# Kernel tuning notes

Hardware: AMD Instinct MI355X
Metric: run time of the kernel (lower is better)

## Reference

```python
import jax, jax.numpy as jnp
import numpy as np

SOFTASSIGN_LAYERS = 10  # MTSPSoftassign layers
EPS = 1e-8


def softassign(output):
    # output: (b, m, n, n)
    b, m, n, _ = output.shape
    # stabilizing max-subtraction (layers > 0 branch)
    depots_max = jnp.max(output[:, :, :1, :], axis=3, keepdims=True)            # (b,m,1,1)
    others_max = jnp.max(output[:, :, 1:, :], axis=(1, 3), keepdims=True)       # (b,1,n-1,1)
    output_max = jnp.concatenate([
        jnp.broadcast_to(depots_max, (b, m, 1, n)),
        jnp.broadcast_to(others_max, (b, m, n - 1, n)),
    ], axis=2)
    output = jnp.exp(output - output_max)
    for _ in range(SOFTASSIGN_LAYERS):
        output = jnp.maximum(output, EPS)
        starts = output[:, :, :1, :]
        starts = starts / jnp.sum(starts, axis=3, keepdims=True)                # normalize_dims (3,)
        nexts = output[:, :, 1:, :]
        nexts = nexts / jnp.sum(nexts, axis=(1, 3), keepdims=True)              # normalize_dims (1,3)
        output = jnp.swapaxes(jnp.concatenate([starts, nexts], axis=2), 2, 3)
    if SOFTASSIGN_LAYERS % 2 != 0:
        output = jnp.swapaxes(output, 2, 3)
    return output


def setup_inputs() -> dict:
    key = jax.random.key(0)
    ks = jax.random.split(key, 4)
    b, m, n, d = 4, 8, 128, 64
    cities = jax.random.normal(ks[0], (b, n, d), dtype=jnp.float32)
    groups = jax.random.normal(ks[1], (b, m, d), dtype=jnp.float32)
    W1 = jax.random.normal(ks[2], (3 * d, d), dtype=jnp.float32) * 0.05
    b1 = jnp.zeros((d,), dtype=jnp.float32)
    W2 = jax.random.normal(ks[3], (d, 1), dtype=jnp.float32) * 0.05
    b2 = jnp.zeros((1,), dtype=jnp.float32)
    return {"cities": cities, "groups": groups, "W1": W1, "b1": b1, "W2": W2, "b2": b2}


def reference(cities, groups, W1, b1, W2, b2):
    # cities: (b, n, d) embedded city features; groups: (b, m, d) embedded group features.
    # Torch builds nodes = cat(at_groups, from_cities, to_cities) of shape (b,m,n,n,3d)
    # then Linear(3d->d). Linear on a concat == sum of linears on the pieces, so we
    # project each piece once and broadcast-add, avoiding the (b,m,n,n,3d) materialization.
    d = cities.shape[-1]
    Wg, Wf, Wt = W1[:d], W1[d:2 * d], W1[2 * d:]
    hg = jnp.einsum('bmd,de->bme', groups, Wg)   # at_groups projection
    hf = jnp.einsum('bnd,de->bne', cities, Wf)   # from_cities projection
    ht = jnp.einsum('bnd,de->bne', cities, Wt)   # to_cities projection
    h = hg[:, :, None, None, :] + hf[:, None, :, None, :] + ht[:, None, None, :, :] + b1  # (b,m,n,n,d)
    h = jax.nn.relu(h)
    out = jnp.einsum('bmfte,eo->bmfto', h, W2)[..., 0] + b2[0]  # (b,m,n,n)
    return softassign(out)
```

## Files before the change

kernel.cpp:

```cpp
#include <hip/hip_runtime.h>
#include <math.h>

#define EPSF 1e-8f

__device__ __forceinline__ void atomicMaxFloat(float* addr, float val) {
    if (val >= 0.f) atomicMax((int*)addr, __float_as_int(val));
    else            atomicMin((unsigned int*)addr, __float_as_uint(val));
}

__global__ __launch_bounds__(256) void prep_kernel(
        const float* __restrict__ cities, const float* __restrict__ groups,
        const float* __restrict__ W1,
        float* __restrict__ hg, float* __restrict__ hf, float* __restrict__ htT,
        float* __restrict__ S, float* __restrict__ Mbuf,
        unsigned* __restrict__ cnt) {
    int blk = blockIdx.x, tid = threadIdx.x;
    if (blk < 128) {
        int gid = blk * 256 + tid;
        int e = gid & 63;
        int f = (gid >> 6) & 127;
        int b = gid >> 13;
        const float* crow = cities + (b * 128 + f) * 64;
        float af = 0.f, at = 0.f;
        #pragma unroll 8
        for (int d = 0; d < 64; ++d) {
            float c = crow[d];
            af = fmaf(c, W1[(64  + d) * 64 + e], af);
            at = fmaf(c, W1[(128 + d) * 64 + e], at);
        }
        hf [(b * 128 + f) * 64 + e] = af;
        htT[(b * 64  + e) * 128 + f] = at;
    } else if (blk < 136) {
        int gid = (blk - 128) * 256 + tid;
        int e = gid & 63;
        int m = (gid >> 6) & 7;
        int b = gid >> 9;
        const float* grow = groups + (b * 8 + m) * 64;
        float a = 0.f;
        #pragma unroll 8
        for (int d = 0; d < 64; ++d)
            a = fmaf(grow[d], W1[d * 64 + e], a);
        hg[(b * 8 + m) * 64 + e] = a;
    } else {
        for (int i = tid; i < 5120; i += 256) S[i] = 0.f;
        for (int i = tid; i < 544;  i += 256) Mbuf[i] = -INFINITY;
        if (tid < 40) cnt[tid] = 0u;
    }
}

__global__ __launch_bounds__(256) void mlp_kernel(
        const float* __restrict__ hg, const float* __restrict__ hf,
        const float* __restrict__ htT,
        const float* __restrict__ b1, const float* __restrict__ W2,
        const float* __restrict__ b2,
        float* __restrict__ X, float* __restrict__ Mdep, float* __restrict__ Moth) {
    int blk = blockIdx.x;
    int fg  = blk & 15;
    int bm  = blk >> 4;
    int b   = bm >> 3;
    int tid = threadIdx.x;

    __shared__ float hts[64][128];
    __shared__ float arowT[64][8];
    __shared__ float w2s[64];
    __shared__ float wmax[4][4];

    {
        const float4* src = (const float4*)(htT + b * 8192);
        float4* dst = (float4*)(&hts[0][0]);
        #pragma unroll
        for (int i = 0; i < 8; ++i) dst[tid + 256 * i] = src[tid + 256 * i];
    }
    #pragma unroll
    for (int j = 0; j < 2; ++j) {
        int v = tid + 256 * j;
        int e = v >> 3, f8 = v & 7;
        int f = fg * 8 + f8;
        arowT[e][f8] = hg[bm * 64 + e] + hf[(b * 128 + f) * 64 + e] + b1[e];
    }
    if (tid < 64) w2s[tid] = W2[tid];
    __syncthreads();

    int t  = tid & 127;
    int fo = tid >> 7;
    float acc[4] = {0.f, 0.f, 0.f, 0.f};
    #pragma unroll 8
    for (int e = 0; e < 64; ++e) {
        float ht = hts[e][t];
        float w2 = w2s[e];
        float4 ar = *(const float4*)(&arowT[e][fo * 4]);
        acc[0] = fmaf(fmaxf(ar.x + ht, 0.f), w2, acc[0]);
        acc[1] = fmaf(fmaxf(ar.y + ht, 0.f), w2, acc[1]);
        acc[2] = fmaf(fmaxf(ar.z + ht, 0.f), w2, acc[2]);
        acc[3] = fmaf(fmaxf(ar.w + ht, 0.f), w2, acc[3]);
    }

    float b2v = b2[0];
    float fmax4[4];
    #pragma unroll
    for (int i = 0; i < 4; ++i) {
        float out = acc[i] + b2v;
        int f = fg * 8 + fo * 4 + i;
        X[(bm * 128 + f) * 128 + t] = out;
        fmax4[i] = out;
    }

    #pragma unroll
    for (int i = 0; i < 4; ++i)
        #pragma unroll
        for (int off = 32; off; off >>= 1)
            fmax4[i] = fmaxf(fmax4[i], __shfl_down(fmax4[i], off));
    int wv = tid >> 6;
    if ((tid & 63) == 0) {
        #pragma unroll
        for (int i = 0; i < 4; ++i) wmax[wv][i] = fmax4[i];
    }
    __syncthreads();
    if (tid < 8) {
        int w0 = (tid >> 2) * 2, i = tid & 3;
        float m = fmaxf(wmax[w0][i], wmax[w0 + 1][i]);
        int f = fg * 8 + tid;
        if (f == 0) atomicMaxFloat(&Mdep[bm], m);
        else        atomicMaxFloat(&Moth[b * 128 + f], m);
    }
}

__global__ __launch_bounds__(1024) void softassign_kernel(
        float* __restrict__ X, const float* __restrict__ Mdep,
        const float* __restrict__ Moth, float* __restrict__ S,
        unsigned* __restrict__ cnt) {
    int blk = blockIdx.x;
    int b = blk >> 3;
    int tid = threadIdx.x;
    int tf = tid >> 5, tt = tid & 31;
    float* base = X + blk * 16384;

    float x[4][4];
    #pragma unroll
    for (int r = 0; r < 4; ++r) {
        float4 v = *(const float4*)(base + (4 * tf + r) * 128 + 4 * tt);
        x[r][0] = v.x; x[r][1] = v.y; x[r][2] = v.z; x[r][3] = v.w;
    }

    float mdep = Mdep[blk];
    #pragma unroll
    for (int r = 0; r < 4; ++r) {
        int f = 4 * tf + r;
        float M = (f == 0) ? mdep : Moth[b * 128 + f];
        #pragma unroll
        for (int c = 0; c < 4; ++c) x[r][c] = expf(x[r][c] - M);
    }

    __shared__ float part[128][33];
    __shared__ float dnm[128];
    __shared__ float depot;

    for (int k = 0; k < 10; ++k) {
        #pragma unroll
        for (int r = 0; r < 4; ++r)
            #pragma unroll
            for (int c = 0; c < 4; ++c) x[r][c] = fmaxf(x[r][c], EPSF);

        int dir = k & 1;
        if (dir == 0) {
            #pragma unroll
            for (int r = 0; r < 4; ++r)
                part[4 * tf + r][tt] = x[r][0] + x[r][1] + x[r][2] + x[r][3];
        } else {
            #pragma unroll
            for (int c = 0; c < 4; ++c)
                part[4 * tt + c][tf] = x[0][c] + x[1][c] + x[2][c] + x[3][c];
        }
        __syncthreads();
        float* Scur = &S[(k * 4 + b) * 128];
        if (tid < 128) {
            float s = 0.f;
            #pragma unroll 8
            for (int j = 0; j < 32; ++j) s += part[tid][j];
            if (tid == 0) depot = s;
            else atomicAdd(&Scur[tid], s);
        }
        __syncthreads();
        unsigned* ccur = &cnt[k * 4 + b];
        if (tid == 0) {
            __hip_atomic_fetch_add(ccur, 1u, __ATOMIC_RELAXED,
                                   __HIP_MEMORY_SCOPE_AGENT);
            while (__hip_atomic_load(ccur, __ATOMIC_RELAXED,
                                     __HIP_MEMORY_SCOPE_AGENT) < 8u)
                __builtin_amdgcn_s_sleep(1);
        }
        __syncthreads();

        if (tid < 128) {
            dnm[tid] = (tid == 0) ? depot
                : __hip_atomic_load(&Scur[tid], __ATOMIC_RELAXED,
                                    __HIP_MEMORY_SCOPE_AGENT);
        }
        __syncthreads();

        if (dir == 0) {
            #pragma unroll
            for (int r = 0; r < 4; ++r) {
                float inv = 1.f / dnm[4 * tf + r];
                #pragma unroll
                for (int c = 0; c < 4; ++c) x[r][c] *= inv;
            }
        } else {
            #pragma unroll
            for (int c = 0; c < 4; ++c) {
                float inv = 1.f / dnm[4 * tt + c];
                #pragma unroll
                for (int r = 0; r < 4; ++r) x[r][c] *= inv;
            }
        }
    }

    #pragma unroll
    for (int r = 0; r < 4; ++r) {
        float4 v = make_float4(x[r][0], x[r][1], x[r][2], x[r][3]);
        *(float4*)(base + (4 * tf + r) * 128 + 4 * tt) = v;
    }
}

extern "C" void kernel_launch(void* const* d_in, const int* in_sizes, int n_in,
                              void* d_out, int out_size, void* d_ws, size_t ws_size,
                              hipStream_t stream) {
    const float* cities = (const float*)d_in[0];
    const float* groups = (const float*)d_in[1];
    const float* W1     = (const float*)d_in[2];
    const float* b1     = (const float*)d_in[3];
    const float* W2     = (const float*)d_in[4];
    const float* b2     = (const float*)d_in[5];
    float* X  = (float*)d_out;
    float* ws = (float*)d_ws;

    float*    hg   = ws;
    float*    hf   = ws + 2048;
    float*    htT  = ws + 34816;
    float*    S    = ws + 67584;
    float*    Mbuf = ws + 72704;
    float*    Mdep = Mbuf;
    float*    Moth = Mbuf + 32;
    unsigned* cnt  = (unsigned*)(ws + 73248);

    prep_kernel<<<137, 256, 0, stream>>>(cities, groups, W1, hg, hf, htT,
                                         S, Mbuf, cnt);
    mlp_kernel<<<512, 256, 0, stream>>>(hg, hf, htT, b1, W2, b2, X, Mdep, Moth);
    softassign_kernel<<<32, 1024, 0, stream>>>(X, Mdep, Moth, S, cnt);
}
```

Before: 103.2 us.

## Replace atomic-add plus counter barrier with per-block slots polled for nonzero

The cross-block column-sum reduction no longer does atomicAdd into a shared sum followed by a counter-based spin barrier. Each of the 8 blocks per batch now stores its partial sums into its own slot. Each thread then polls all 8 slots until every one is nonzero and sums them locally, which removes the atomic contention and the extra barrier round. To support this, the workspace is enlarged and zeroed by more prep blocks using float4 stores. The approach relies on partial sums never being exactly zero, which holds because entries are clamped to at least EPS.

```diff
diff --git a/kernel.cpp b/kernel.cpp
--- a/kernel.cpp
+++ b/kernel.cpp
@@ -12,8 +12,7 @@
         const float* __restrict__ cities, const float* __restrict__ groups,
         const float* __restrict__ W1,
         float* __restrict__ hg, float* __restrict__ hf, float* __restrict__ htT,
-        float* __restrict__ S, float* __restrict__ Mbuf,
-        unsigned* __restrict__ cnt) {
+        float* __restrict__ S, float* __restrict__ Mbuf) {
     int blk = blockIdx.x, tid = threadIdx.x;
     if (blk < 128) {
         int gid = blk * 256 + tid;
@@ -42,9 +41,15 @@
             a = fmaf(grow[d], W1[d * 64 + e], a);
         hg[(b * 8 + m) * 64 + e] = a;
     } else {
-        for (int i = tid; i < 5120; i += 256) S[i] = 0.f;
-        for (int i = tid; i < 544;  i += 256) Mbuf[i] = -INFINITY;
-        if (tid < 40) cnt[tid] = 0u;
+        int zb = blk - 136;
+        float4 z = make_float4(0.f, 0.f, 0.f, 0.f);
+        float4* S4 = (float4*)S;
+        #pragma unroll
+        for (int i = 0; i < 5; ++i) S4[zb * 1280 + 256 * i + tid] = z;
+        if (zb == 7 && tid < 136) {
+            float ninf = -INFINITY;
+            ((float4*)Mbuf)[tid] = make_float4(ninf, ninf, ninf, ninf);
+        }
     }
 }
 
@@ -127,10 +132,9 @@
 
 __global__ __launch_bounds__(1024) void softassign_kernel(
         float* __restrict__ X, const float* __restrict__ Mdep,
-        const float* __restrict__ Moth, float* __restrict__ S,
-        unsigned* __restrict__ cnt) {
+        const float* __restrict__ Moth, float* __restrict__ S) {
     int blk = blockIdx.x;
-    int b = blk >> 3;
+    int b = blk >> 3, m = blk & 7;
     int tid = threadIdx.x;
     int tf = tid >> 5, tt = tid & 31;
     float* base = X + blk * 16384;
@@ -153,7 +157,6 @@
 
     __shared__ float part[128][33];
     __shared__ float dnm[128];
-    __shared__ float depot;
 
     for (int k = 0; k < 10; ++k) {
         #pragma unroll
@@ -172,29 +175,34 @@
                 part[4 * tt + c][tf] = x[0][c] + x[1][c] + x[2][c] + x[3][c];
         }
         __syncthreads();
-        float* Scur = &S[(k * 4 + b) * 128];
         if (tid < 128) {
             float s = 0.f;
             #pragma unroll 8
             for (int j = 0; j < 32; ++j) s += part[tid][j];
-            if (tid == 0) depot = s;
-            else atomicAdd(&Scur[tid], s);
-        }
-        __syncthreads();
-        unsigned* ccur = &cnt[k * 4 + b];
-        if (tid == 0) {
-            __hip_atomic_fetch_add(ccur, 1u, __ATOMIC_RELAXED,
-                                   __HIP_MEMORY_SCOPE_AGENT);
-            while (__hip_atomic_load(ccur, __ATOMIC_RELAXED,
-                                     __HIP_MEMORY_SCOPE_AGENT) < 8u)
-                __builtin_amdgcn_s_sleep(1);
-        }
-        __syncthreads();
-
-        if (tid < 128) {
-            dnm[tid] = (tid == 0) ? depot
-                : __hip_atomic_load(&Scur[tid], __ATOMIC_RELAXED,
-                                    __HIP_MEMORY_SCOPE_AGENT);
+            if (tid == 0) {
+                dnm[0] = s;
+            } else {
+                float* Scur = S + (k * 4 + b) * 1024;
+                __hip_atomic_store(&Scur[m * 128 + tid], s,
+                                   __ATOMIC_RELAXED, __HIP_MEMORY_SCOPE_AGENT);
+                float tot;
+                for (;;) {
+                    float v[8]; bool ready = true;
+                    #pragma unroll
+                    for (int j = 0; j < 8; ++j)
+                        v[j] = __hip_atomic_load(&Scur[j * 128 + tid],
+                                 __ATOMIC_RELAXED, __HIP_MEMORY_SCOPE_AGENT);
+                    #pragma unroll
+                    for (int j = 0; j < 8; ++j) ready &= (v[j] != 0.f);
+                    if (ready) {
+                        tot = ((v[0] + v[1]) + (v[2] + v[3]))
+                            + ((v[4] + v[5]) + (v[6] + v[7]));
+                        break;
+                    }
+                    __builtin_amdgcn_s_sleep(1);
+                }
+                dnm[tid] = tot;
+            }
         }
         __syncthreads();
 
@@ -234,17 +242,16 @@
     float* X  = (float*)d_out;
     float* ws = (float*)d_ws;
 
-    float*    hg   = ws;
-    float*    hf   = ws + 2048;
-    float*    htT  = ws + 34816;
-    float*    S    = ws + 67584;
-    float*    Mbuf = ws + 72704;
-    float*    Mdep = Mbuf;
-    float*    Moth = Mbuf + 32;
-    unsigned* cnt  = (unsigned*)(ws + 73248);
-
-    prep_kernel<<<137, 256, 0, stream>>>(cities, groups, W1, hg, hf, htT,
-                                         S, Mbuf, cnt);
+    float* hg   = ws;
+    float* hf   = ws + 2048;
+    float* htT  = ws + 34816;
+    float* S    = ws + 67584;
+    float* Mbuf = ws + 108544;
+    float* Mdep = Mbuf;
+    float* Moth = Mbuf + 32;
+
+    prep_kernel<<<144, 256, 0, stream>>>(cities, groups, W1, hg, hf, htT,
+                                         S, Mbuf);
     mlp_kernel<<<512, 256, 0, stream>>>(hg, hf, htT, b1, W2, b2, X, Mdep, Moth);
-    softassign_kernel<<<32, 1024, 0, stream>>>(X, Mdep, Moth, S, cnt);
-}
+    softassign_kernel<<<32, 1024, 0, stream>>>(X, Mdep, Moth, S);
+}
```

New measurement: 99.10 us. -4.0%, faster.

## Reformulate softassign as Sinkhorn scaling vectors over compressed column sums

Applied to the files above, without the earlier changes.

Sinkhorn normalization is rewritten as per-row and per-column scaling factors. Only reduced summaries of exp(X) enter the iterations: column sums over m for non-depot rows, plus the depot row and column per group. A single block per batch runs the ten iterations entirely in shared memory, and a final scale kernel applies the factors to X. This removes the max-subtraction atomics, the cross-block spin-wait barriers and the per-iteration global atomics. In exchange it drops the max stabilization and the EPS clamp, which risks overflow or a change in numerics on other inputs.

```diff
diff --git a/kernel.cpp b/kernel.cpp
--- a/kernel.cpp
+++ b/kernel.cpp
@@ -1,19 +1,10 @@
 #include <hip/hip_runtime.h>
 #include <math.h>
-
-#define EPSF 1e-8f
-
-__device__ __forceinline__ void atomicMaxFloat(float* addr, float val) {
-    if (val >= 0.f) atomicMax((int*)addr, __float_as_int(val));
-    else            atomicMin((unsigned int*)addr, __float_as_uint(val));
-}
 
 __global__ __launch_bounds__(256) void prep_kernel(
         const float* __restrict__ cities, const float* __restrict__ groups,
         const float* __restrict__ W1,
-        float* __restrict__ hg, float* __restrict__ hf, float* __restrict__ htT,
-        float* __restrict__ S, float* __restrict__ Mbuf,
-        unsigned* __restrict__ cnt) {
+        float* __restrict__ hg, float* __restrict__ hf, float* __restrict__ htT) {
     int blk = blockIdx.x, tid = threadIdx.x;
     if (blk < 128) {
         int gid = blk * 256 + tid;
@@ -30,7 +21,7 @@
         }
         hf [(b * 128 + f) * 64 + e] = af;
         htT[(b * 64  + e) * 128 + f] = at;
-    } else if (blk < 136) {
+    } else {
         int gid = (blk - 128) * 256 + tid;
         int e = gid & 63;
         int m = (gid >> 6) & 7;
@@ -41,10 +32,6 @@
         for (int d = 0; d < 64; ++d)
             a = fmaf(grow[d], W1[d * 64 + e], a);
         hg[(b * 8 + m) * 64 + e] = a;
-    } else {
-        for (int i = tid; i < 5120; i += 256) S[i] = 0.f;
-        for (int i = tid; i < 544;  i += 256) Mbuf[i] = -INFINITY;
-        if (tid < 40) cnt[tid] = 0u;
     }
 }
 
@@ -53,7 +40,7 @@
         const float* __restrict__ htT,
         const float* __restrict__ b1, const float* __restrict__ W2,
         const float* __restrict__ b2,
-        float* __restrict__ X, float* __restrict__ Mdep, float* __restrict__ Moth) {
+        float* __restrict__ X) {
     int blk = blockIdx.x;
     int fg  = blk & 15;
     int bm  = blk >> 4;
@@ -63,7 +50,6 @@
     __shared__ float hts[64][128];
     __shared__ float arowT[64][8];
     __shared__ float w2s[64];
-    __shared__ float wmax[4][4];
 
     {
         const float4* src = (const float4*)(htT + b * 8192);
@@ -96,130 +82,149 @@
     }
 
     float b2v = b2[0];
-    float fmax4[4];
     #pragma unroll
     for (int i = 0; i < 4; ++i) {
-        float out = acc[i] + b2v;
         int f = fg * 8 + fo * 4 + i;
-        X[(bm * 128 + f) * 128 + t] = out;
-        fmax4[i] = out;
-    }
-
-    #pragma unroll
-    for (int i = 0; i < 4; ++i)
+        X[(bm * 128 + f) * 128 + t] = expf(acc[i] + b2v);
+    }
+}
+
+__global__ __launch_bounds__(1024) void softassign_kernel(
+        const float* __restrict__ X, float* __restrict__ Fac) {
+    int b   = blockIdx.x;
+    int tid = threadIdx.x;
+    int f = tid >> 3, c = tid & 7;
+
+    __shared__ float CS[128][129];
+    __shared__ float R0[8][128];
+    __shared__ float C0[8][128];
+    __shared__ float F[128], G[128];
+    __shared__ float Fm[8], G0m[8];
+
+    const float* bbase = X + b * 131072;
+    float cs[16];
+    #pragma unroll
+    for (int j = 0; j < 16; ++j) cs[j] = 0.f;
+    #pragma unroll
+    for (int m = 0; m < 8; ++m) {
+        const float4* src = (const float4*)(bbase + (m * 128 + f) * 128 + c * 16);
+        float4 v0 = src[0], v1 = src[1], v2 = src[2], v3 = src[3];
+        cs[0]  += v0.x; cs[1]  += v0.y; cs[2]  += v0.z; cs[3]  += v0.w;
+        cs[4]  += v1.x; cs[5]  += v1.y; cs[6]  += v1.z; cs[7]  += v1.w;
+        cs[8]  += v2.x; cs[9]  += v2.y; cs[10] += v2.z; cs[11] += v2.w;
+        cs[12] += v3.x; cs[13] += v3.y; cs[14] += v3.z; cs[15] += v3.w;
+        if (f == 0) {
+            float4* r = (float4*)(&R0[m][c * 16]);
+            r[0] = v0; r[1] = v1; r[2] = v2; r[3] = v3;
+        }
+        if (c == 0) C0[m][f] = v0.x;
+    }
+    if (c == 0) cs[0] = 0.f;
+    if (f == 0) {
         #pragma unroll
-        for (int off = 32; off; off >>= 1)
-            fmax4[i] = fmaxf(fmax4[i], __shfl_down(fmax4[i], off));
-    int wv = tid >> 6;
-    if ((tid & 63) == 0) {
+        for (int j = 0; j < 16; ++j) CS[0][c * 16 + j] = 0.f;
+    } else {
         #pragma unroll
-        for (int i = 0; i < 4; ++i) wmax[wv][i] = fmax4[i];
-    }
+        for (int j = 0; j < 16; ++j) CS[f][c * 16 + j] = cs[j];
+    }
+    if (tid < 128) G[tid] = (tid == 0) ? 0.f : 1.f;
+    if (tid == 0) F[0] = 0.f;
+    if (tid >= 128 && tid < 136) { Fm[tid - 128] = 1.f; G0m[tid - 128] = 1.f; }
     __syncthreads();
-    if (tid < 8) {
-        int w0 = (tid >> 2) * 2, i = tid & 3;
-        float m = fmaxf(wmax[w0][i], wmax[w0 + 1][i]);
-        int f = fg * 8 + tid;
-        if (f == 0) atomicMaxFloat(&Mdep[bm], m);
-        else        atomicMaxFloat(&Moth[b * 128 + f], m);
-    }
-}
-
-__global__ __launch_bounds__(1024) void softassign_kernel(
-        float* __restrict__ X, const float* __restrict__ Mdep,
-        const float* __restrict__ Moth, float* __restrict__ S,
-        unsigned* __restrict__ cnt) {
-    int blk = blockIdx.x;
-    int b = blk >> 3;
-    int tid = threadIdx.x;
-    int tf = tid >> 5, tt = tid & 31;
-    float* base = X + blk * 16384;
-
-    float x[4][4];
-    #pragma unroll
-    for (int r = 0; r < 4; ++r) {
-        float4 v = *(const float4*)(base + (4 * tf + r) * 128 + 4 * tt);
-        x[r][0] = v.x; x[r][1] = v.y; x[r][2] = v.z; x[r][3] = v.w;
-    }
-
-    float mdep = Mdep[blk];
-    #pragma unroll
-    for (int r = 0; r < 4; ++r) {
-        int f = 4 * tf + r;
-        float M = (f == 0) ? mdep : Moth[b * 128 + f];
-        #pragma unroll
-        for (int c = 0; c < 4; ++c) x[r][c] = expf(x[r][c] - M);
-    }
-
-    __shared__ float part[128][33];
-    __shared__ float dnm[128];
-    __shared__ float depot;
 
     for (int k = 0; k < 10; ++k) {
-        #pragma unroll
-        for (int r = 0; r < 4; ++r)
+        if (!(k & 1)) {
+            float p = 0.f;
             #pragma unroll
-            for (int c = 0; c < 4; ++c) x[r][c] = fmaxf(x[r][c], EPSF);
-
-        int dir = k & 1;
-        if (dir == 0) {
+            for (int j = 0; j < 16; ++j)
+                p = fmaf(G[c * 16 + j], CS[f][c * 16 + j], p);
+            if (c == 0) {
+                #pragma unroll
+                for (int m = 0; m < 8; ++m) p = fmaf(G0m[m], C0[m][f], p);
+            }
+            p += __shfl_xor(p, 1); p += __shfl_xor(p, 2); p += __shfl_xor(p, 4);
+            if (c == 0 && f > 0) F[f] = 1.f / p;
+            if (f == 0) {
+                float pm[8];
+                #pragma unroll
+                for (int m = 0; m < 8; ++m) {
+                    float s = 0.f;
+                    #pragma unroll
+                    for (int j = 0; j < 16; ++j) {
+                        float cf = (c == 0 && j == 0) ? G0m[m] : G[c * 16 + j];
+                        s = fmaf(cf, R0[m][c * 16 + j], s);
+                    }
+                    pm[m] = s;
+                }
+                #pragma unroll
+                for (int m = 0; m < 8; ++m) {
+                    pm[m] += __shfl_xor(pm[m], 1);
+                    pm[m] += __shfl_xor(pm[m], 2);
+                    pm[m] += __shfl_xor(pm[m], 4);
+                }
+                Fm[c] = 1.f / pm[c];
+            }
+        } else {
+            int tt = f, rc = c;
+            float p = 0.f;
             #pragma unroll
-            for (int r = 0; r < 4; ++r)
-                part[4 * tf + r][tt] = x[r][0] + x[r][1] + x[r][2] + x[r][3];
-        } else {
-            #pragma unroll
-            for (int c = 0; c < 4; ++c)
-                part[4 * tt + c][tf] = x[0][c] + x[1][c] + x[2][c] + x[3][c];
+            for (int u = 0; u < 16; ++u)
+                p = fmaf(F[rc * 16 + u], CS[rc * 16 + u][tt], p);
+            if (rc == 0) {
+                #pragma unroll
+                for (int m = 0; m < 8; ++m) p = fmaf(Fm[m], R0[m][tt], p);
+            }
+            p += __shfl_xor(p, 1); p += __shfl_xor(p, 2); p += __shfl_xor(p, 4);
+            if (rc == 0 && tt > 0) G[tt] = 1.f / p;
+            if (tt == 0) {
+                float qm[8];
+                #pragma unroll
+                for (int m = 0; m < 8; ++m) {
+                    float s = 0.f;
+                    #pragma unroll
+                    for (int u = 0; u < 16; ++u) {
+                        float rf = (rc == 0 && u == 0) ? Fm[m] : F[rc * 16 + u];
+                        s = fmaf(rf, C0[m][rc * 16 + u], s);
+                    }
+                    qm[m] = s;
+                }
+                #pragma unroll
+                for (int m = 0; m < 8; ++m) {
+                    qm[m] += __shfl_xor(qm[m], 1);
+                    qm[m] += __shfl_xor(qm[m], 2);
+                    qm[m] += __shfl_xor(qm[m], 4);
+                }
+                G0m[rc] = 1.f / qm[rc];
+            }
         }
         __syncthreads();
-        float* Scur = &S[(k * 4 + b) * 128];
-        if (tid < 128) {
-            float s = 0.f;
-            #pragma unroll 8
-            for (int j = 0; j < 32; ++j) s += part[tid][j];
-            if (tid == 0) depot = s;
-            else atomicAdd(&Scur[tid], s);
-        }
-        __syncthreads();
-        unsigned* ccur = &cnt[k * 4 + b];
-        if (tid == 0) {
-            __hip_atomic_fetch_add(ccur, 1u, __ATOMIC_RELAXED,
-                                   __HIP_MEMORY_SCOPE_AGENT);
-            while (__hip_atomic_load(ccur, __ATOMIC_RELAXED,
-                                     __HIP_MEMORY_SCOPE_AGENT) < 8u)
-                __builtin_amdgcn_s_sleep(1);
-        }
-        __syncthreads();
-
-        if (tid < 128) {
-            dnm[tid] = (tid == 0) ? depot
-                : __hip_atomic_load(&Scur[tid], __ATOMIC_RELAXED,
-                                    __HIP_MEMORY_SCOPE_AGENT);
-        }
-        __syncthreads();
-
-        if (dir == 0) {
-            #pragma unroll
-            for (int r = 0; r < 4; ++r) {
-                float inv = 1.f / dnm[4 * tf + r];
-                #pragma unroll
-                for (int c = 0; c < 4; ++c) x[r][c] *= inv;
-            }
-        } else {
-            #pragma unroll
-            for (int c = 0; c < 4; ++c) {
-                float inv = 1.f / dnm[4 * tt + c];
-                #pragma unroll
-                for (int r = 0; r < 4; ++r) x[r][c] *= inv;
-            }
-        }
-    }
-
-    #pragma unroll
-    for (int r = 0; r < 4; ++r) {
-        float4 v = make_float4(x[r][0], x[r][1], x[r][2], x[r][3]);
-        *(float4*)(base + (4 * tf + r) * 128 + 4 * tt) = v;
-    }
+    }
+
+    float* fb = Fac + b * 272;
+    if (tid < 128)       fb[tid] = F[tid];
+    else if (tid < 136)  fb[tid] = Fm[tid - 128];
+    else if (tid < 264)  fb[tid] = G[tid - 136];
+    else if (tid < 272)  fb[tid] = G0m[tid - 264];
+}
+
+__global__ __launch_bounds__(256) void scale_kernel(
+        float* __restrict__ X, const float* __restrict__ Fac) {
+    int blk = blockIdx.x;
+    int bm = blk >> 4, fg = blk & 15;
+    int b = bm >> 3, m = bm & 7;
+    int tid = threadIdx.x;
+    int f  = fg * 8 + (tid >> 5);
+    int t0 = (tid & 31) * 4;
+
+    const float* fb = Fac + b * 272;
+    float rf = (f == 0) ? fb[128 + m] : fb[f];
+    float4 g = *(const float4*)(fb + 136 + t0);
+    if (t0 == 0) g.x = fb[264 + m];
+
+    float* p = X + (bm * 128 + f) * 128 + t0;
+    float4 v = *(float4*)p;
+    v.x *= rf * g.x; v.y *= rf * g.y; v.z *= rf * g.z; v.w *= rf * g.w;
+    *(float4*)p = v;
 }
 
 extern "C" void kernel_launch(void* const* d_in, const int* in_sizes, int n_in,
@@ -234,17 +239,13 @@
     float* X  = (float*)d_out;
     float* ws = (float*)d_ws;
 
-    float*    hg   = ws;
-    float*    hf   = ws + 2048;
-    float*    htT  = ws + 34816;
-    float*    S    = ws + 67584;
-    float*    Mbuf = ws + 72704;
-    float*    Mdep = Mbuf;
-    float*    Moth = Mbuf + 32;
-    unsigned* cnt  = (unsigned*)(ws + 73248);
-
-    prep_kernel<<<137, 256, 0, stream>>>(cities, groups, W1, hg, hf, htT,
-                                         S, Mbuf, cnt);
-    mlp_kernel<<<512, 256, 0, stream>>>(hg, hf, htT, b1, W2, b2, X, Mdep, Moth);
-    softassign_kernel<<<32, 1024, 0, stream>>>(X, Mdep, Moth, S, cnt);
-}
+    float* hg  = ws;
+    float* hf  = ws + 2048;
+    float* htT = ws + 34816;
+    float* Fac = ws + 67584;
+
+    prep_kernel<<<136, 256, 0, stream>>>(cities, groups, W1, hg, hf, htT);
+    mlp_kernel<<<512, 256, 0, stream>>>(hg, hf, htT, b1, W2, b2, X);
+    softassign_kernel<<<4, 1024, 0, stream>>>(X, Fac);
+    scale_kernel<<<512, 256, 0, stream>>>(X, Fac);
+}
```

After: 108.6 us. 1.05x slower.
